# Kernel optimization log

Measured on AMD Instinct MI355X. Metric: run time of the kernel, lower is better.

The kernel has to match this reference:

```python
import jax, jax.numpy as jnp
import numpy as np

IMG, P, CIN, D, K, L, H, FF, B = 512, 32, 3, 256, 8192, 6, 8, 1024, 32
GRID = IMG // P  # 16
DH = D // H
EPS = 1e-5


def _ln(x, w, b):
    m = x.mean(-1, keepdims=True)
    v = ((x - m) ** 2).mean(-1, keepdims=True)
    return (x - m) / jnp.sqrt(v + EPS) * w + b


def _mha(x, wqkv, bqkv, wo, bo):
    # x: (S, Bt, D) -- axis 0 is the attention axis (torch batch_first=False quirk)
    S, Bt, _ = x.shape
    qkv = x @ wqkv.T + bqkv
    q, k, v = jnp.split(qkv, 3, axis=-1)
    q = q.reshape(S, Bt, H, DH)
    k = k.reshape(S, Bt, H, DH)
    v = v.reshape(S, Bt, H, DH)
    scores = jnp.einsum('sbhd,tbhd->bhst', q, k) / jnp.sqrt(jnp.float32(DH))
    attn = jax.nn.softmax(scores, axis=-1)
    o = jnp.einsum('bhst,tbhd->sbhd', attn, v).reshape(S, Bt, D)
    return o @ wo.T + bo


def _conv_t(x, w, b, stride=2, pad=1):
    # w uses torch ConvTranspose2d layout (Cin, Cout, kH, kW)
    kH = w.shape[2]
    wf = jnp.flip(w, (2, 3)).transpose(1, 0, 2, 3)  # -> (Cout, Cin, kH, kW)
    y = jax.lax.conv_general_dilated(
        x, wf, window_strides=(1, 1),
        padding=[(kH - 1 - pad, kH - 1 - pad)] * 2,
        lhs_dilation=(stride, stride),
        dimension_numbers=('NCHW', 'OIHW', 'NCHW'))
    return y + b[None, :, None, None]


def _forward(x, patch_w, patch_b, qkv_w, qkv_b, out_w, out_b, ln1_w, ln1_b,
             ln2_w, ln2_b, ff1_w, ff1_b, ff2_w, ff2_b, lnf_w, lnf_b, codebook,
             dec_w0, dec_b0, dec_w1, dec_b1, dec_w2, dec_b2, dec_w3, dec_b3):
    # patch embedding: conv stride=patch -> (B, D, G, G) -> (B, N, D)
    h = jax.lax.conv_general_dilated(
        x, patch_w, (P, P), 'VALID',
        dimension_numbers=('NCHW', 'OIHW', 'NCHW')) + patch_b[None, :, None, None]
    h = h.reshape(h.shape[0], D, -1).transpose(0, 2, 1)  # (B, N, D)
    # torch TransformerEncoderLayer default batch_first=False: attention runs
    # over axis 0 (image batch); faithfully replicated here. Post-norm, eval
    # mode (dropout=identity), exact gelu.
    for i in range(L):
        a = _mha(h, qkv_w[i], qkv_b[i], out_w[i], out_b[i])
        h = _ln(h + a, ln1_w[i], ln1_b[i])
        f = jax.nn.gelu(h @ ff1_w[i].T + ff1_b[i], approximate=False) @ ff2_w[i].T + ff2_b[i]
        h = _ln(h + f, ln2_w[i], ln2_b[i])
    h = _ln(h, lnf_w, lnf_b)
    # vector quantization: squared-distance argmin over codebook
    flat = h.reshape(-1, D)  # (B*N, D)
    d = ((flat ** 2).sum(-1, keepdims=True)
         - 2.0 * flat @ codebook.T
         + (codebook ** 2).sum(-1))  # (B*N, K)
    idx = jnp.argmin(d, axis=1)
    q = codebook[idx].reshape(h.shape)
    e_loss = jnp.mean((jax.lax.stop_gradient(q) - h) ** 2)
    q_loss = jnp.mean((q - jax.lax.stop_gradient(h)) ** 2)
    vq_loss = q_loss + 0.25 * e_loss
    q = h + jax.lax.stop_gradient(q - h)  # straight-through
    q = q.transpose(0, 2, 1).reshape(x.shape[0], D, GRID, GRID)
    y = jax.nn.relu(_conv_t(q, dec_w0, dec_b0))
    y = jax.nn.relu(_conv_t(y, dec_w1, dec_b1))
    y = jax.nn.relu(_conv_t(y, dec_w2, dec_b2))
    x_hat = jax.nn.sigmoid(_conv_t(y, dec_w3, dec_b3))
    return x_hat, vq_loss


def setup_inputs() -> dict:
    key = jax.random.key(0)
    ks = iter(jax.random.split(key, 64))
    nrm = lambda shape, s=0.02: jax.random.normal(next(ks), shape, jnp.float32) * s
    f32 = jnp.float32
    return {
        'x': jax.random.normal(next(ks), (B, CIN, IMG, IMG), f32),
        'patch_w': nrm((D, CIN, P, P)),
        'patch_b': jnp.zeros((D,), f32),
        'qkv_w': nrm((L, 3 * D, D)),
        'qkv_b': jnp.zeros((L, 3 * D), f32),
        'out_w': nrm((L, D, D)),
        'out_b': jnp.zeros((L, D), f32),
        'ln1_w': jnp.ones((L, D), f32),
        'ln1_b': jnp.zeros((L, D), f32),
        'ln2_w': jnp.ones((L, D), f32),
        'ln2_b': jnp.zeros((L, D), f32),
        'ff1_w': nrm((L, FF, D)),
        'ff1_b': jnp.zeros((L, FF), f32),
        'ff2_w': nrm((L, D, FF)),
        'ff2_b': jnp.zeros((L, D), f32),
        'lnf_w': jnp.ones((D,), f32),
        'lnf_b': jnp.zeros((D,), f32),
        'codebook': jax.random.uniform(next(ks), (K, D), f32, -1.0 / K, 1.0 / K),
        'dec_w0': nrm((D, 256, 4, 4)),
        'dec_b0': jnp.zeros((256,), f32),
        'dec_w1': nrm((256, 128, 4, 4)),
        'dec_b1': jnp.zeros((128,), f32),
        'dec_w2': nrm((128, 64, 4, 4)),
        'dec_b2': jnp.zeros((64,), f32),
        'dec_w3': nrm((64, CIN, 4, 4)),
        'dec_b3': jnp.zeros((CIN,), f32),
    }


def reference(x, patch_w, patch_b, qkv_w, qkv_b, out_w, out_b, ln1_w, ln1_b,
              ln2_w, ln2_b, ff1_w, ff1_b, ff2_w, ff2_b, lnf_w, lnf_b, codebook,
              dec_w0, dec_b0, dec_w1, dec_b1, dec_w2, dec_b2, dec_w3, dec_b3):
    return _forward(x, patch_w, patch_b, qkv_w, qkv_b, out_w, out_b, ln1_w,
                    ln1_b, ln2_w, ln2_b, ff1_w, ff1_b, ff2_w, ff2_b, lnf_w,
                    lnf_b, codebook, dec_w0, dec_b0, dec_w1, dec_b1, dec_w2,
                    dec_b2, dec_w3, dec_b3)
```

## Files before the change

### kernel.cpp

```cpp
#include <hip/hip_runtime.h>
#include <hip/hip_bf16.h>
#include <math.h>

typedef __hip_bfloat16 bf16;
typedef unsigned int u32;
typedef unsigned long long u64;
using short8 = __attribute__((ext_vector_type(8))) short;
using f32x4  = __attribute__((ext_vector_type(4))) float;

__device__ __forceinline__ float b2f(bf16 v){ return __bfloat162float(v); }
__device__ __forceinline__ bf16  f2b(float v){ return __float2bfloat16(v); }
__device__ __forceinline__ float plo(u32 u){ return __uint_as_float(u << 16); }
__device__ __forceinline__ float phi(u32 u){ return __uint_as_float(u & 0xffff0000u); }

__device__ __forceinline__ void gld16(const void* g, void* l)
{
  __builtin_amdgcn_global_load_lds(
      (const __attribute__((address_space(1))) u32*)g,
      (__attribute__((address_space(3))) u32*)l, 16, 0, 0);
}

__global__ void k_detect(const u32* probe, int* flag)
{
  if (threadIdx.x == 0 && blockIdx.x == 0)
    *flag = (*probe == 0x3F800000u) ? 0 : 1;
}

struct PPack { const void* s[25]; u32 off[26]; };
__global__ __launch_bounds__(256) void k_convall(PPack pp, bf16* P, const int* flag)
{
  const u32 i = blockIdx.x * 256 + threadIdx.x;
  if (i >= pp.off[25]) return;
  int lo = 0, hi = 25;
  while (hi - lo > 1) { const int mid = (lo + hi) >> 1; if (i >= pp.off[mid]) lo = mid; else hi = mid; }
  const u32 j = i - pp.off[lo];
  P[i] = *flag ? ((const bf16*)pp.s[lo])[j] : f2b(((const float*)pp.s[lo])[j]);
}

__global__ __launch_bounds__(256) void k_zero(u32* p, int n)
{
  const int i = blockIdx.x * 256 + threadIdx.x;
  if (i < n) p[i] = 0;
}

__global__ __launch_bounds__(128) void k_im2col(const void* x, bf16* A, const int* flag)
{
  const int m = blockIdx.y;
  const int k8 = blockIdx.x * 128 + threadIdx.x;
  const int k = k8 * 8;
  const int b = m >> 8, n = m & 255;
  const int gy = n >> 4, gx = n & 15;
  const int c = k >> 10, r = (k >> 5) & 31, pp = k & 31;
  const size_t src = (((size_t)(b * 3 + c) * 512) + gy * 32 + r) * 512 + gx * 32 + pp;
  bf16 ov[8];
  if (*flag) {
    const bf16* xp = (const bf16*)x + src;
    #pragma unroll
    for (int i = 0; i < 8; ++i) ov[i] = xp[i];
  } else {
    const float4 v0 = *reinterpret_cast<const float4*>((const float*)x + src);
    const float4 v1 = *reinterpret_cast<const float4*>((const float*)x + src + 4);
    ov[0]=f2b(v0.x); ov[1]=f2b(v0.y); ov[2]=f2b(v0.z); ov[3]=f2b(v0.w);
    ov[4]=f2b(v1.x); ov[5]=f2b(v1.y); ov[6]=f2b(v1.z); ov[7]=f2b(v1.w);
  }
  *reinterpret_cast<uint4*>(A + (size_t)m * 3072 + k) = *reinterpret_cast<const uint4*>(ov);
}

template<int EPI, int FM, bool DB>
__global__ __launch_bounds__(256, 2) void gemm_t(
    const bf16* __restrict__ A, const bf16* __restrict__ Bw,
    const bf16* __restrict__ bias, const bf16* res, bf16* C, float* __restrict__ Cf,
    const float* __restrict__ cnorm, u64* __restrict__ ku,
    int M, int N, int K, int Kc)
{
  constexpr int BM = FM * 32;
  __shared__ alignas(16) bf16 As[DB ? 2 : 1][BM * 64];
  __shared__ alignas(16) bf16 Bs[DB ? 2 : 1][128 * 64];
  const int tid = threadIdx.x;
  const int bn = blockIdx.x * 128, bm = blockIdx.y * BM;
  const int z = blockIdx.z;
  const int kb = z * Kc;
  const int l = tid & 63, w = tid >> 6;
  const int wm = w >> 1, wn = w & 1;
  const int lg = l >> 4, lr = l & 15;
  const int sr8 = l >> 3;
  const int sch = (l & 7) ^ sr8;
  f32x4 acc[FM][4];
  #pragma unroll
  for (int fm = 0; fm < FM; ++fm)
    #pragma unroll
    for (int fn = 0; fn < 4; ++fn) acc[fm][fn] = (f32x4){0.f, 0.f, 0.f, 0.f};

  auto stage = [&](int bb, int k0) {
    char* ab = (char*)As[bb];
    char* bp = (char*)Bs[bb];
    #pragma unroll
    for (int it = 0; it < FM; ++it) {
      const int r = w * 8 + it * 32 + sr8;
      gld16(A + (size_t)(bm + r) * K + k0 + sch * 8, ab + w * 1024 + it * 4096);
    }
    #pragma unroll
    for (int it = 0; it < 4; ++it) {
      const int r = w * 8 + it * 32 + sr8;
      gld16(Bw + (size_t)(bn + r) * K + k0 + sch * 8, bp + w * 1024 + it * 4096);
    }
  };
  auto compute = [&](int bb) {
    const char* ab = (const char*)As[bb];
    const char* bp = (const char*)Bs[bb];
    #pragma unroll
    for (int ks = 0; ks < 2; ++ks) {
      short8 af[FM], bfr[4];
      #pragma unroll
      for (int fm = 0; fm < FM; ++fm) {
        const int r = wm * (FM * 16) + fm * 16 + lr;
        af[fm] = *reinterpret_cast<const short8*>(ab + r * 128 + (((lg + ks * 4) ^ (r & 7)) * 16));
      }
      #pragma unroll
      for (int fn = 0; fn < 4; ++fn) {
        const int r = wn * 64 + fn * 16 + lr;
        bfr[fn] = *reinterpret_cast<const short8*>(bp + r * 128 + (((lg + ks * 4) ^ (r & 7)) * 16));
      }
      #pragma unroll
      for (int fm = 0; fm < FM; ++fm)
        #pragma unroll
        for (int fn = 0; fn < 4; ++fn)
          acc[fm][fn] = __builtin_amdgcn_mfma_f32_16x16x32_bf16(af[fm], bfr[fn], acc[fm][fn], 0, 0, 0);
    }
  };

  const int nt = Kc >> 6;
  if (DB) {
    stage(0, kb);
    __syncthreads();
    for (int t = 0; t < nt; ++t) {
      const int cur = t & 1;
      if (t + 1 < nt) stage(cur ^ 1, kb + ((t + 1) << 6));
      compute(cur);
      __syncthreads();
    }
  } else {
    for (int t = 0; t < nt; ++t) {
      if (t) __syncthreads();
      stage(0, kb + (t << 6));
      __syncthreads();
      compute(0);
    }
  }

  if (EPI == 3) {
    __shared__ u64 skey[BM][2];
    float cn4[4];
    #pragma unroll
    for (int fn = 0; fn < 4; ++fn) cn4[fn] = cnorm[bn + wn * 64 + fn * 16 + lr];
    #pragma unroll
    for (int fm = 0; fm < FM; ++fm) {
      #pragma unroll
      for (int r = 0; r < 4; ++r) {
        u64 best = ~0ull;
        #pragma unroll
        for (int fn = 0; fn < 4; ++fn) {
          const int col = bn + wn * 64 + fn * 16 + lr;
          const float d = cn4[fn] - 2.0f * acc[fm][fn][r];
          u32 u = __float_as_uint(d);
          u = (u & 0x80000000u) ? ~u : (u | 0x80000000u);
          const u64 key = ((u64)u << 32) | (u32)col;
          best = key < best ? key : best;
        }
        #pragma unroll
        for (int mk = 1; mk < 16; mk <<= 1) {
          const u64 o = __shfl_xor(best, mk, 64);
          best = o < best ? o : best;
        }
        if (lr == 0) skey[wm * (FM * 16) + fm * 16 + lg * 4 + r][wn] = best;
      }
    }
    __syncthreads();
    if (tid < BM) {
      const u64 a = skey[tid][0], b = skey[tid][1];
      ku[(size_t)blockIdx.x * M + bm + tid] = a < b ? a : b;
    }
  } else if (EPI == 4) {
    #pragma unroll
    for (int fm = 0; fm < FM; ++fm) {
      const int m0 = bm + wm * (FM * 16) + fm * 16 + lg * 4;
      #pragma unroll
      for (int fn = 0; fn < 4; ++fn) {
        const int n = bn + wn * 64 + fn * 16 + lr;
        #pragma unroll
        for (int r = 0; r < 4; ++r)
          Cf[((size_t)z * M + m0 + r) * N + n] = acc[fm][fn][r];
      }
    }
  } else {
    #pragma unroll
    for (int fm = 0; fm < FM; ++fm) {
      const int m0 = bm + wm * (FM * 16) + fm * 16 + lg * 4;
      #pragma unroll
      for (int fn = 0; fn < 4; ++fn) {
        const int n = bn + wn * 64 + fn * 16 + lr;
        const float bs = b2f(bias[n]);
        #pragma unroll
        for (int r = 0; r < 4; ++r) {
          float v = acc[fm][fn][r] + bs;
          if (EPI == 1) v = 0.5f * v * (1.0f + erff(v * 0.70710678118654752f));
          if (EPI == 2) v += b2f(res[(size_t)(m0 + r) * N + n]);
          C[(size_t)(m0 + r) * N + n] = f2b(v);
        }
      }
    }
  }
}

template<bool DOLN>
__global__ __launch_bounds__(256) void k_lnred(
    const float* __restrict__ Pf, const bf16* __restrict__ bias,
    const bf16* res, const bf16* __restrict__ lw, const bf16* __restrict__ lb,
    bf16* h, int kc)
{
  __shared__ float red[256];
  __shared__ float stat[2];
  const int row = blockIdx.x, d = threadIdx.x;
  float s = 0.f;
  for (int z = 0; z < kc; ++z) s += Pf[((size_t)z * 8192 + row) * 256 + d];
  s += b2f(bias[d]);
  if (res) s += b2f(res[(size_t)row * 256 + d]);
  if (!DOLN) { h[(size_t)row * 256 + d] = f2b(s); return; }
  red[d] = s;
  __syncthreads();
  for (int off = 128; off > 0; off >>= 1) {
    if (d < off) red[d] += red[d + off];
    __syncthreads();
  }
  if (d == 0) stat[0] = red[0] * (1.0f / 256.0f);
  __syncthreads();
  const float m = stat[0];
  red[d] = (s - m) * (s - m);
  __syncthreads();
  for (int off = 128; off > 0; off >>= 1) {
    if (d < off) red[d] += red[d + off];
    __syncthreads();
  }
  if (d == 0) stat[1] = 1.0f / sqrtf(red[0] * (1.0f / 256.0f) + 1e-5f);
  __syncthreads();
  h[(size_t)row * 256 + d] = f2b((s - m) * stat[1] * b2f(lw[d]) + b2f(lb[d]));
}

__global__ __launch_bounds__(256) void k_vqmerge(
    const u64* __restrict__ ku, int* __restrict__ idx, int M, int NB)
{
  const int r = blockIdx.x * 256 + threadIdx.x;
  if (r >= M) return;
  u64 best = ku[r];
  for (int nb = 1; nb < NB; ++nb) {
    const u64 k = ku[(size_t)nb * M + r];
    best = k < best ? k : best;
  }
  idx[r] = (int)(best & 0xFFFFFFFFull);
}

__global__ __launch_bounds__(256) void k_cnorm(const bf16* __restrict__ cb, float* __restrict__ cn)
{
  const int j = blockIdx.x * 256 + threadIdx.x;
  const u32* p = (const u32*)(cb + (size_t)j * 256);
  float s = 0.f;
  for (int k = 0; k < 128; ++k) {
    const u32 v = p[k];
    const float a = plo(v), b = phi(v);
    s += a * a + b * b;
  }
  cn[j] = s;
}

__global__ __launch_bounds__(256) void k_ln(
    bf16* h, const bf16* w, const bf16* b)
{
  __shared__ float red[256];
  __shared__ float stat[2];
  const int row = blockIdx.x, d = threadIdx.x;
  const size_t base = (size_t)row * 256;
  const float x = b2f(h[base + d]);
  red[d] = x;
  __syncthreads();
  for (int off = 128; off > 0; off >>= 1) {
    if (d < off) red[d] += red[d + off];
    __syncthreads();
  }
  if (d == 0) stat[0] = red[0] * (1.0f / 256.0f);
  __syncthreads();
  const float m = stat[0];
  red[d] = (x - m) * (x - m);
  __syncthreads();
  for (int off = 128; off > 0; off >>= 1) {
    if (d < off) red[d] += red[d + off];
    __syncthreads();
  }
  if (d == 0) stat[1] = 1.0f / sqrtf(red[0] * (1.0f / 256.0f) + 1e-5f);
  __syncthreads();
  h[base + d] = f2b((x - m) * stat[1] * b2f(w[d]) + b2f(b[d]));
}

__global__ __launch_bounds__(256) void k_attn(
    const bf16* __restrict__ qkv, bf16* __restrict__ o)
{
  __shared__ float qs[32][33], ks[32][33], vs[32][33], ps[32][33];
  __shared__ float rs[32];
  const int bt = blockIdx.x, hd = blockIdx.y;
  const int tid = threadIdx.x;
  #pragma unroll
  for (int e = 0; e < 2; ++e) {
    const int i = tid + 256 * e;
    if (i < 384) {
      const int plane = i >> 7;
      const int rem = i & 127;
      const int s = rem >> 2, c4 = rem & 3;
      const uint4 v = *reinterpret_cast<const uint4*>(
          qkv + (size_t)(s * 256 + bt) * 768 + plane * 256 + hd * 32 + c4 * 8);
      float* dst = (plane == 0 ? &qs[s][0] : plane == 1 ? &ks[s][0] : &vs[s][0]) + c4 * 8;
      dst[0]=plo(v.x); dst[1]=phi(v.x); dst[2]=plo(v.y); dst[3]=phi(v.y);
      dst[4]=plo(v.z); dst[5]=phi(v.z); dst[6]=plo(v.w); dst[7]=phi(v.w);
    }
  }
  __syncthreads();
  const int s = tid >> 3, j = tid & 7;
  float sc[4];
  #pragma unroll
  for (int e = 0; e < 4; ++e) {
    const int t = j + 8 * e;
    float v = 0.f;
    #pragma unroll
    for (int dd = 0; dd < 32; ++dd) v += qs[s][dd] * ks[t][dd];
    sc[e] = v * 0.17677669529663687f;
  }
  float mx = fmaxf(fmaxf(sc[0], sc[1]), fmaxf(sc[2], sc[3]));
  #pragma unroll
  for (int mk = 1; mk < 8; mk <<= 1) mx = fmaxf(mx, __shfl_xor(mx, mk, 64));
  float sm = 0.f; float ex[4];
  #pragma unroll
  for (int e = 0; e < 4; ++e) { ex[e] = expf(sc[e] - mx); sm += ex[e]; }
  #pragma unroll
  for (int mk = 1; mk < 8; mk <<= 1) sm += __shfl_xor(sm, mk, 64);
  #pragma unroll
  for (int e = 0; e < 4; ++e) ps[s][j + 8 * e] = ex[e];
  if (j == 0) rs[s] = 1.0f / sm;
  __syncthreads();
  const float rinv = rs[s];
  float av[4];
  #pragma unroll
  for (int e = 0; e < 4; ++e) {
    const int dd = j * 4 + e;
    float acc = 0.f;
    #pragma unroll
    for (int t = 0; t < 32; ++t) acc += ps[s][t] * vs[t][dd];
    av[e] = acc * rinv;
  }
  alignas(8) bf16 ov[4];
  #pragma unroll
  for (int e = 0; e < 4; ++e) ov[e] = f2b(av[e]);
  *reinterpret_cast<ushort4*>(o + (size_t)(s * 256 + bt) * 256 + hd * 32 + j * 4) =
      *reinterpret_cast<const ushort4*>(ov);
}

__global__ __launch_bounds__(256) void k_gather(
    const bf16* h, const bf16* cb, const int* idx, bf16* a0, float* lsum)
{
  __shared__ float red[256];
  const int row = blockIdx.x, d = threadIdx.x;
  const int code = idx[row] & 8191;
  const float q = b2f(cb[(size_t)code * 256 + d]);
  const float x = b2f(h[(size_t)row * 256 + d]);
  red[d] = (q - x) * (q - x);
  __syncthreads();
  for (int off = 128; off > 0; off >>= 1) {
    if (d < off) red[d] += red[d + off];
    __syncthreads();
  }
  if (d == 0) lsum[row] = red[0];
  const int b = row >> 8, n = row & 255;
  const int y = n >> 4, xc = n & 15;
  a0[(((size_t)b * 18 + y + 1) * 18 + (xc + 1)) * 256 + d] = f2b(q);
}

__global__ __launch_bounds__(256) void k_loss(const float* lsum, float* out)
{
  __shared__ float red[256];
  const int tid = threadIdx.x;
  float v = 0.f;
  for (int i = 0; i < 32; ++i) v += lsum[tid + 256 * i];
  red[tid] = v;
  __syncthreads();
  for (int off = 128; off > 0; off >>= 1) {
    if (tid < off) red[tid] += red[tid + off];
    __syncthreads();
  }
  if (tid == 0)
    out[0] = red[0] * (1.25f / 2097152.0f);
}

__global__ __launch_bounds__(256) void k_wtrans(
    const bf16* __restrict__ w, bf16* __restrict__ wt,
    int Cin, int lCin, int CoutR, int CoutP)
{
  const int K = Cin << 2;
  const int total = 4 * CoutP * K;
  const int i = blockIdx.x * 256 + threadIdx.x;
  if (i >= total) return;
  const int p = i / (CoutP * K);
  const int rem = i - p * (CoutP * K);
  const int co = rem / K;
  const int k = rem - co * K;
  const int tap = k >> lCin, ci = k - (tap << lCin);
  const int py = p >> 1, px = p & 1, ty = tap >> 1, tx = tap & 1;
  bf16 v = f2b(0.f);
  if (co < CoutR)
    v = w[(((size_t)ci * CoutR + co) * 4 + py + 2 * ty) * 4 + px + 2 * tx];
  wt[i] = v;
}

__global__ __launch_bounds__(256, 2) void convt64(
    const bf16* __restrict__ in, const bf16* __restrict__ Wt,
    const bf16* __restrict__ bias, bf16* __restrict__ outp,
    int H, int lH, int Cin, int lCin, int Cout)
{
  __shared__ alignas(16) bf16 As[2][128 * 64];
  __shared__ alignas(16) bf16 Bs[2][64 * 64];
  const int tid = threadIdx.x;
  const int pz = blockIdx.z;
  const int py = pz >> 1, px = pz & 1;
  const int K = Cin << 2;
  const int bn = blockIdx.x * 64, bm = blockIdx.y * 128;
  const bf16* Bw = Wt + (size_t)pz * Cout * K;
  const int l = tid & 63, w = tid >> 6;
  const int wm = w >> 1, wn = w & 1;
  const int lg = l >> 4, lr = l & 15;
  const int sr8 = l >> 3;
  const int sch = (l & 7) ^ sr8;
  const int Hp = H + 2;
  f32x4 acc[4][2];
  #pragma unroll
  for (int fm = 0; fm < 4; ++fm)
    #pragma unroll
    for (int fn = 0; fn < 2; ++fn) acc[fm][fn] = (f32x4){0.f, 0.f, 0.f, 0.f};

  size_t pixbase[4];
  #pragma unroll
  for (int it = 0; it < 4; ++it) {
    const int m = bm + w * 8 + it * 32 + sr8;
    const int b = m >> (2 * lH);
    const int rem = m & ((1 << (2 * lH)) - 1);
    const int jj = rem >> lH, ii = rem & (H - 1);
    pixbase[it] = ((size_t)(b * Hp + jj) * Hp + ii);
  }

  auto stage = [&](int bb, int k0) {
    char* ab = (char*)As[bb];
    char* bp = (char*)Bs[bb];
    const int tap = k0 >> lCin;
    const int ty = tap >> 1, tx = tap & 1;
    const int sy = (1 - py) + (1 - ty);
    const int sx = (1 - px) + (1 - tx);
    const int ci0 = (k0 - (tap << lCin)) + sch * 8;
    #pragma unroll
    for (int it = 0; it < 4; ++it)
      gld16(in + (pixbase[it] + (size_t)sy * Hp + sx) * Cin + ci0,
            ab + w * 1024 + it * 4096);
    #pragma unroll
    for (int it = 0; it < 2; ++it) {
      const int r = w * 8 + it * 32 + sr8;
      gld16(Bw + (size_t)(bn + r) * K + k0 + sch * 8, bp + w * 1024 + it * 4096);
    }
  };

  const int nt = K >> 6;
  stage(0, 0);
  __syncthreads();
  for (int t = 0; t < nt; ++t) {
    const int cur = t & 1;
    if (t + 1 < nt) stage(cur ^ 1, (t + 1) << 6);
    const char* ab = (const char*)As[cur];
    const char* bb = (const char*)Bs[cur];
    #pragma unroll
    for (int ks = 0; ks < 2; ++ks) {
      short8 af[4], bfr[2];
      #pragma unroll
      for (int fm = 0; fm < 4; ++fm) {
        const int r = wm * 64 + fm * 16 + lr;
        af[fm] = *reinterpret_cast<const short8*>(ab + r * 128 + (((lg + ks * 4) ^ (r & 7)) * 16));
      }
      #pragma unroll
      for (int fn = 0; fn < 2; ++fn) {
        const int r = wn * 32 + fn * 16 + lr;
        bfr[fn] = *reinterpret_cast<const short8*>(bb + r * 128 + (((lg + ks * 4) ^ (r & 7)) * 16));
      }
      #pragma unroll
      for (int fm = 0; fm < 4; ++fm)
        #pragma unroll
        for (int fn = 0; fn < 2; ++fn)
          acc[fm][fn] = __builtin_amdgcn_mfma_f32_16x16x32_bf16(af[fm], bfr[fn], acc[fm][fn], 0, 0, 0);
    }
    __syncthreads();
  }

  const int Ho = 2 * H, Hop = Ho + 2;
  #pragma unroll
  for (int fm = 0; fm < 4; ++fm) {
    const int m0 = bm + wm * 64 + fm * 16 + lg * 4;
    #pragma unroll
    for (int fn = 0; fn < 2; ++fn) {
      const int n = bn + wn * 32 + fn * 16 + lr;
      #pragma unroll
      for (int r = 0; r < 4; ++r) {
        const int m = m0 + r;
        const int b = m >> (2 * lH);
        const int rem = m & ((1 << (2 * lH)) - 1);
        const int jj = rem >> lH, ii = rem & (H - 1);
        const int oy = 2 * jj + (1 - py), ox = 2 * ii + (1 - px);
        const float v = fmaxf(acc[fm][fn][r] + b2f(bias[n]), 0.f);
        outp[((size_t)(b * Hop + oy + 1) * Hop + ox + 1) * Cout + n] = f2b(v);
      }
    }
  }
}

__global__ __launch_bounds__(256) void k_dec3(
    const bf16* __restrict__ a3, const bf16* __restrict__ wt3,
    const bf16* __restrict__ bias, float* __restrict__ xhat, int chunkBase)
{
  __shared__ float wl[3][264];
  const int tid = threadIdx.x;
  const int pz = blockIdx.y;
  const int py = pz >> 1, px = pz & 1;
  for (int i = tid; i < 768; i += 256) {
    const int co = i >> 8, k = i & 255;
    wl[co][k] = b2f(wt3[(pz * 3 + co) * 256 + k]);
  }
  __syncthreads();
  const int b = blockIdx.z;
  const int p = blockIdx.x * 64 + (tid >> 2);
  const int jj = p >> 7, ii = p & 127;
  const int ch4 = tid & 3;
  float a0 = 0.f, a1 = 0.f, a2 = 0.f;
  #pragma unroll
  for (int ty = 0; ty < 2; ++ty) {
    #pragma unroll
    for (int tx = 0; tx < 2; ++tx) {
      const int sy = (1 - py) + (1 - ty), sx = (1 - px) + (1 - tx);
      const int tap = ty * 2 + tx;
      const u32* ip = (const u32*)(a3 + ((size_t)(b * 130 + jj + sy) * 130 + ii + sx) * 64) + ch4 * 8;
      const float* w0 = &wl[0][tap * 64 + ch4 * 16];
      const float* w1 = &wl[1][tap * 64 + ch4 * 16];
      const float* w2 = &wl[2][tap * 64 + ch4 * 16];
      #pragma unroll
      for (int kk = 0; kk < 8; ++kk) {
        const u32 v = ip[kk];
        const float e0 = plo(v), e1 = phi(v);
        a0 += e0 * w0[2 * kk] + e1 * w0[2 * kk + 1];
        a1 += e0 * w1[2 * kk] + e1 * w1[2 * kk + 1];
        a2 += e0 * w2[2 * kk] + e1 * w2[2 * kk + 1];
      }
    }
  }
  a0 += __shfl_xor(a0, 1, 64); a0 += __shfl_xor(a0, 2, 64);
  a1 += __shfl_xor(a1, 1, 64); a1 += __shfl_xor(a1, 2, 64);
  a2 += __shfl_xor(a2, 1, 64); a2 += __shfl_xor(a2, 2, 64);
  if (ch4 < 3) {
    const float av = ch4 == 0 ? a0 : (ch4 == 1 ? a1 : a2);
    const int oy = 2 * jj + (1 - py), ox = 2 * ii + (1 - px);
    const float t = av + b2f(bias[ch4]);
    xhat[(((size_t)(chunkBase + b) * 3 + ch4) * 256 + oy) * 256 + ox] =
        1.0f / (1.0f + expf(-t));
  }
}

extern "C" void kernel_launch(void* const* d_in, const int* in_sizes, int n_in,
                              void* d_out, int out_size, void* d_ws, size_t ws_size,
                              hipStream_t stream)
{
  float* xhat = (float*)d_out;
  float* lossout = xhat + (out_size - 1);

  const size_t NEED = 130195456;
  if (ws_size < NEED) return;

  char* ws = (char*)d_ws;
  int*   flag  = (int*)  (ws + 0);
  float* lsum  = (float*)(ws + 1024);
  int*   idx   = (int*)  (ws + 65536);
  u64*   ku    = (u64*)  (ws + 131072);
  bf16*  P     = (bf16*) (ws + 8519680);
  bf16*  WT    = (bf16*) (ws + 27262976);
  float* cnorm = (float*)(ws + 30900224);
  bf16*  hbuf  = (bf16*) (ws + 31457280);
  bf16*  A_im  = (bf16*) (ws + 35651584);
  bf16*  qkvb  = (bf16*) (ws + 35651584);
  bf16*  obuf  = (bf16*) (ws + 48234496);
  bf16*  ffb   = (bf16*) (ws + 52428800);
  float* Pf    = (float*)(ws + 85983232);
  bf16*  a0    = (bf16*) (ws + 35651584);
  bf16*  a1    = (bf16*) (ws + 40960000);
  bf16*  a2    = (bf16*) (ws + 59899904);
  bf16*  a3    = (bf16*) (ws + 95584256);

  k_detect<<<1, 64, 0, stream>>>((const u32*)d_in[7], flag);

  size_t poff[26]; poff[1] = 0;
  for (int i = 2; i <= 25; ++i) poff[i] = poff[i - 1] + (size_t)in_sizes[i - 1];
  const size_t ptotal = poff[25] + (size_t)in_sizes[25];
  PPack pp;
  for (int i = 0; i < 25; ++i) { pp.s[i] = d_in[i + 1]; pp.off[i] = (u32)poff[i + 1]; }
  pp.off[25] = (u32)ptotal;
  k_convall<<<(int)((ptotal + 255) / 256), 256, 0, stream>>>(pp, P, flag);

  const bf16 *patch_w = P + poff[1],  *patch_b = P + poff[2];
  const bf16 *qkv_w   = P + poff[3],  *qkv_b   = P + poff[4];
  const bf16 *out_w   = P + poff[5],  *out_b   = P + poff[6];
  const bf16 *ln1_w   = P + poff[7],  *ln1_b   = P + poff[8];
  const bf16 *ln2_w   = P + poff[9],  *ln2_b   = P + poff[10];
  const bf16 *ff1_w   = P + poff[11], *ff1_b   = P + poff[12];
  const bf16 *ff2_w   = P + poff[13], *ff2_b   = P + poff[14];
  const bf16 *lnf_w   = P + poff[15], *lnf_b   = P + poff[16];
  const bf16 *codebook= P + poff[17];
  const bf16 *dec_w0  = P + poff[18], *dec_b0  = P + poff[19];
  const bf16 *dec_w1  = P + poff[20], *dec_b1  = P + poff[21];
  const bf16 *dec_w2  = P + poff[22], *dec_b2  = P + poff[23];
  const bf16 *dec_w3  = P + poff[24], *dec_b3  = P + poff[25];

  bf16* wt0 = WT;
  bf16* wt1 = wt0 + 1048576;
  bf16* wt2 = wt1 + 524288;
  bf16* wt3 = wt2 + 131072;
  k_wtrans<<<(1048576 + 255) / 256, 256, 0, stream>>>(dec_w0, wt0, 256, 8, 256, 256);
  k_wtrans<<<(524288 + 255) / 256, 256, 0, stream>>>(dec_w1, wt1, 256, 8, 128, 128);
  k_wtrans<<<(131072 + 255) / 256, 256, 0, stream>>>(dec_w2, wt2, 128, 7, 64, 64);
  k_wtrans<<<(3072 + 255) / 256, 256, 0, stream>>>(dec_w3, wt3, 64, 6, 3, 3);
  k_cnorm<<<32, 256, 0, stream>>>(codebook, cnorm);

  k_im2col<<<dim3(3, 8192), 128, 0, stream>>>(d_in[0], A_im, flag);
  gemm_t<4, 2, true><<<dim3(2, 128, 4), 256, 0, stream>>>(
      A_im, patch_w, nullptr, nullptr, nullptr, Pf, nullptr, nullptr, 8192, 256, 3072, 768);
  k_lnred<false><<<8192, 256, 0, stream>>>(
      Pf, patch_b, nullptr, nullptr, nullptr, hbuf, 4);

  for (int l = 0; l < 6; ++l) {
    gemm_t<0, 2, false><<<dim3(6, 128, 1), 256, 0, stream>>>(
        hbuf, qkv_w + (size_t)l * 768 * 256, qkv_b + l * 768, nullptr, qkvb, nullptr,
        nullptr, nullptr, 8192, 768, 256, 256);
    k_attn<<<dim3(256, 8), 256, 0, stream>>>(qkvb, obuf);
    gemm_t<2, 2, false><<<dim3(2, 128, 1), 256, 0, stream>>>(
        obuf, out_w + (size_t)l * 256 * 256, out_b + l * 256, hbuf, hbuf, nullptr,
        nullptr, nullptr, 8192, 256, 256, 256);
    k_ln<<<8192, 256, 0, stream>>>(hbuf, ln1_w + l * 256, ln1_b + l * 256);
    gemm_t<1, 2, false><<<dim3(8, 128, 1), 256, 0, stream>>>(
        hbuf, ff1_w + (size_t)l * 1024 * 256, ff1_b + l * 1024, nullptr, ffb, nullptr,
        nullptr, nullptr, 8192, 1024, 256, 256);
    gemm_t<4, 2, false><<<dim3(2, 128, 4), 256, 0, stream>>>(
        ffb, ff2_w + (size_t)l * 256 * 1024, nullptr, nullptr, nullptr, Pf,
        nullptr, nullptr, 8192, 256, 1024, 256);
    k_lnred<true><<<8192, 256, 0, stream>>>(
        Pf, ff2_b + l * 256, hbuf, ln2_w + l * 256, ln2_b + l * 256, hbuf, 4);
  }
  k_ln<<<8192, 256, 0, stream>>>(hbuf, lnf_w, lnf_b);

  gemm_t<3, 2, false><<<dim3(64, 128, 1), 256, 0, stream>>>(
      hbuf, codebook, nullptr, nullptr, nullptr, nullptr, cnorm, ku, 8192, 8192, 256, 256);
  k_vqmerge<<<32, 256, 0, stream>>>(ku, idx, 8192, 64);

  k_zero<<<(1327104 + 255) / 256, 256, 0, stream>>>((u32*)a0, 1327104);
  k_gather<<<8192, 256, 0, stream>>>(hbuf, codebook, idx, a0, lsum);
  k_loss<<<1, 256, 0, stream>>>(lsum, lossout);

  k_zero<<<(4734976 + 255) / 256, 256, 0, stream>>>((u32*)a1, 4734976);
  k_zero<<<(8921088 + 255) / 256, 256, 0, stream>>>((u32*)a2, 8921088);
  k_zero<<<(8652800 + 255) / 256, 256, 0, stream>>>((u32*)a3, 8652800);

  convt64<<<dim3(4, 64, 4), 256, 0, stream>>>(a0, wt0, dec_b0, a1, 16, 4, 256, 8, 256);
  convt64<<<dim3(2, 256, 4), 256, 0, stream>>>(a1, wt1, dec_b1, a2, 32, 5, 256, 8, 128);
  for (int c = 0; c < 2; ++c) {
    const bf16* a2c = a2 + (size_t)c * 16 * 66 * 66 * 128;
    convt64<<<dim3(1, 512, 4), 256, 0, stream>>>(a2c, wt2, dec_b2, a3, 64, 6, 128, 7, 64);
    k_dec3<<<dim3(256, 4, 16), 256, 0, stream>>>(a3, wt3, dec_b3, xhat, c * 16);
  }
}
```

Baseline: 1.019 ms.

## Zero only padding borders, store split-K partials in bf16, widen GEMM N tiles

Full-buffer zeroing of the padded decoder activations is replaced by a kernel that writes zeros only to the one-pixel border, assuming the interior is fully overwritten. Split-K partial sums for the patch embedding and FF2 GEMMs are now stored in bf16 instead of fp32, halving that write and reread traffic at some cost in accumulation precision. The GEMM gains a BN template parameter, and the QKV, FF1 and VQ-distance GEMMs use 256-wide N tiles, which halves their grid size and doubles per-block accumulator registers.

```diff
diff --git a/kernel.cpp b/kernel.cpp
--- a/kernel.cpp
+++ b/kernel.cpp
@@ -37,10 +37,28 @@
   P[i] = *flag ? ((const bf16*)pp.s[lo])[j] : f2b(((const float*)pp.s[lo])[j]);
 }
 
-__global__ __launch_bounds__(256) void k_zero(u32* p, int n)
-{
+__global__ __launch_bounds__(256) void k_zborder(bf16* buf, int Hp, int C, int nimg)
+{
+  const int per = 4 * Hp - 4;
+  const int c8 = C >> 3;
+  const int total = nimg * per * c8;
   const int i = blockIdx.x * 256 + threadIdx.x;
-  if (i < n) p[i] = 0;
+  if (i >= total) return;
+  const int ch8 = i % c8;
+  const int pb = i / c8;
+  const int img = pb / per;
+  const int b = pb - img * per;
+  int y, x;
+  if (b < Hp) { y = 0; x = b; }
+  else if (b < 2 * Hp) { y = Hp - 1; x = b - Hp; }
+  else {
+    const int r = b - 2 * Hp;
+    const int side = r / (Hp - 2);
+    y = 1 + r - side * (Hp - 2);
+    x = side ? (Hp - 1) : 0;
+  }
+  uint4 z = {0, 0, 0, 0};
+  *reinterpret_cast<uint4*>(buf + (((size_t)img * Hp + y) * Hp + x) * C + ch8 * 8) = z;
 }
 
 __global__ __launch_bounds__(128) void k_im2col(const void* x, bf16* A, const int* flag)
@@ -66,18 +84,19 @@
   *reinterpret_cast<uint4*>(A + (size_t)m * 3072 + k) = *reinterpret_cast<const uint4*>(ov);
 }
 
-template<int EPI, int FM, bool DB>
+template<int EPI, int FM, int BN, bool DB>
 __global__ __launch_bounds__(256, 2) void gemm_t(
     const bf16* __restrict__ A, const bf16* __restrict__ Bw,
-    const bf16* __restrict__ bias, const bf16* res, bf16* C, float* __restrict__ Cf,
+    const bf16* __restrict__ bias, const bf16* res, bf16* C,
     const float* __restrict__ cnorm, u64* __restrict__ ku,
     int M, int N, int K, int Kc)
 {
   constexpr int BM = FM * 32;
+  constexpr int FN = BN / 32;
   __shared__ alignas(16) bf16 As[DB ? 2 : 1][BM * 64];
-  __shared__ alignas(16) bf16 Bs[DB ? 2 : 1][128 * 64];
+  __shared__ alignas(16) bf16 Bs[DB ? 2 : 1][BN * 64];
   const int tid = threadIdx.x;
-  const int bn = blockIdx.x * 128, bm = blockIdx.y * BM;
+  const int bn = blockIdx.x * BN, bm = blockIdx.y * BM;
   const int z = blockIdx.z;
   const int kb = z * Kc;
   const int l = tid & 63, w = tid >> 6;
@@ -85,11 +104,11 @@
   const int lg = l >> 4, lr = l & 15;
   const int sr8 = l >> 3;
   const int sch = (l & 7) ^ sr8;
-  f32x4 acc[FM][4];
+  f32x4 acc[FM][FN];
   #pragma unroll
   for (int fm = 0; fm < FM; ++fm)
     #pragma unroll
-    for (int fn = 0; fn < 4; ++fn) acc[fm][fn] = (f32x4){0.f, 0.f, 0.f, 0.f};
+    for (int fn = 0; fn < FN; ++fn) acc[fm][fn] = (f32x4){0.f, 0.f, 0.f, 0.f};
 
   auto stage = [&](int bb, int k0) {
     char* ab = (char*)As[bb];
@@ -100,7 +119,7 @@
       gld16(A + (size_t)(bm + r) * K + k0 + sch * 8, ab + w * 1024 + it * 4096);
     }
     #pragma unroll
-    for (int it = 0; it < 4; ++it) {
+    for (int it = 0; it < BN / 32; ++it) {
       const int r = w * 8 + it * 32 + sr8;
       gld16(Bw + (size_t)(bn + r) * K + k0 + sch * 8, bp + w * 1024 + it * 4096);
     }
@@ -110,21 +129,21 @@
     const char* bp = (const char*)Bs[bb];
     #pragma unroll
     for (int ks = 0; ks < 2; ++ks) {
-      short8 af[FM], bfr[4];
+      short8 af[FM], bfr[FN];
       #pragma unroll
       for (int fm = 0; fm < FM; ++fm) {
         const int r = wm * (FM * 16) + fm * 16 + lr;
         af[fm] = *reinterpret_cast<const short8*>(ab + r * 128 + (((lg + ks * 4) ^ (r & 7)) * 16));
       }
       #pragma unroll
-      for (int fn = 0; fn < 4; ++fn) {
-        const int r = wn * 64 + fn * 16 + lr;
+      for (int fn = 0; fn < FN; ++fn) {
+        const int r = wn * (BN / 2) + fn * 16 + lr;
         bfr[fn] = *reinterpret_cast<const short8*>(bp + r * 128 + (((lg + ks * 4) ^ (r & 7)) * 16));
       }
       #pragma unroll
       for (int fm = 0; fm < FM; ++fm)
         #pragma unroll
-        for (int fn = 0; fn < 4; ++fn)
+        for (int fn = 0; fn < FN; ++fn)
           acc[fm][fn] = __builtin_amdgcn_mfma_f32_16x16x32_bf16(af[fm], bfr[fn], acc[fm][fn], 0, 0, 0);
     }
   };
@@ -150,18 +169,18 @@
 
   if (EPI == 3) {
     __shared__ u64 skey[BM][2];
-    float cn4[4];
-    #pragma unroll
-    for (int fn = 0; fn < 4; ++fn) cn4[fn] = cnorm[bn + wn * 64 + fn * 16 + lr];
+    float cn[FN];
+    #pragma unroll
+    for (int fn = 0; fn < FN; ++fn) cn[fn] = cnorm[bn + wn * (BN / 2) + fn * 16 + lr];
     #pragma unroll
     for (int fm = 0; fm < FM; ++fm) {
       #pragma unroll
       for (int r = 0; r < 4; ++r) {
         u64 best = ~0ull;
         #pragma unroll
-        for (int fn = 0; fn < 4; ++fn) {
-          const int col = bn + wn * 64 + fn * 16 + lr;
-          const float d = cn4[fn] - 2.0f * acc[fm][fn][r];
+        for (int fn = 0; fn < FN; ++fn) {
+          const int col = bn + wn * (BN / 2) + fn * 16 + lr;
+          const float d = cn[fn] - 2.0f * acc[fm][fn][r];
           u32 u = __float_as_uint(d);
           u = (u & 0x80000000u) ? ~u : (u | 0x80000000u);
           const u64 key = ((u64)u << 32) | (u32)col;
@@ -185,11 +204,11 @@
     for (int fm = 0; fm < FM; ++fm) {
       const int m0 = bm + wm * (FM * 16) + fm * 16 + lg * 4;
       #pragma unroll
-      for (int fn = 0; fn < 4; ++fn) {
-        const int n = bn + wn * 64 + fn * 16 + lr;
+      for (int fn = 0; fn < FN; ++fn) {
+        const int n = bn + wn * (BN / 2) + fn * 16 + lr;
         #pragma unroll
         for (int r = 0; r < 4; ++r)
-          Cf[((size_t)z * M + m0 + r) * N + n] = acc[fm][fn][r];
+          C[((size_t)z * M + m0 + r) * N + n] = f2b(acc[fm][fn][r]);
       }
     }
   } else {
@@ -197,8 +216,8 @@
     for (int fm = 0; fm < FM; ++fm) {
       const int m0 = bm + wm * (FM * 16) + fm * 16 + lg * 4;
       #pragma unroll
-      for (int fn = 0; fn < 4; ++fn) {
-        const int n = bn + wn * 64 + fn * 16 + lr;
+      for (int fn = 0; fn < FN; ++fn) {
+        const int n = bn + wn * (BN / 2) + fn * 16 + lr;
         const float bs = b2f(bias[n]);
         #pragma unroll
         for (int r = 0; r < 4; ++r) {
@@ -214,7 +233,7 @@
 
 template<bool DOLN>
 __global__ __launch_bounds__(256) void k_lnred(
-    const float* __restrict__ Pf, const bf16* __restrict__ bias,
+    const bf16* __restrict__ Pf, const bf16* __restrict__ bias,
     const bf16* res, const bf16* __restrict__ lw, const bf16* __restrict__ lb,
     bf16* h, int kc)
 {
@@ -222,7 +241,7 @@
   __shared__ float stat[2];
   const int row = blockIdx.x, d = threadIdx.x;
   float s = 0.f;
-  for (int z = 0; z < kc; ++z) s += Pf[((size_t)z * 8192 + row) * 256 + d];
+  for (int z = 0; z < kc; ++z) s += b2f(Pf[((size_t)z * 8192 + row) * 256 + d]);
   s += b2f(bias[d]);
   if (res) s += b2f(res[(size_t)row * 256 + d]);
   if (!DOLN) { h[(size_t)row * 256 + d] = f2b(s); return; }
@@ -595,7 +614,7 @@
   bf16*  qkvb  = (bf16*) (ws + 35651584);
   bf16*  obuf  = (bf16*) (ws + 48234496);
   bf16*  ffb   = (bf16*) (ws + 52428800);
-  float* Pf    = (float*)(ws + 85983232);
+  bf16*  Pfb   = (bf16*) (ws + 85983232);
   bf16*  a0    = (bf16*) (ws + 35651584);
   bf16*  a1    = (bf16*) (ws + 40960000);
   bf16*  a2    = (bf16*) (ws + 59899904);
@@ -636,42 +655,41 @@
   k_cnorm<<<32, 256, 0, stream>>>(codebook, cnorm);
 
   k_im2col<<<dim3(3, 8192), 128, 0, stream>>>(d_in[0], A_im, flag);
-  gemm_t<4, 2, true><<<dim3(2, 128, 4), 256, 0, stream>>>(
-      A_im, patch_w, nullptr, nullptr, nullptr, Pf, nullptr, nullptr, 8192, 256, 3072, 768);
+  gemm_t<4, 2, 128, true><<<dim3(2, 128, 4), 256, 0, stream>>>(
+      A_im, patch_w, nullptr, nullptr, Pfb, nullptr, nullptr, 8192, 256, 3072, 768);
   k_lnred<false><<<8192, 256, 0, stream>>>(
-      Pf, patch_b, nullptr, nullptr, nullptr, hbuf, 4);
+      Pfb, patch_b, nullptr, nullptr, nullptr, hbuf, 4);
 
   for (int l = 0; l < 6; ++l) {
-    gemm_t<0, 2, false><<<dim3(6, 128, 1), 256, 0, stream>>>(
-        hbuf, qkv_w + (size_t)l * 768 * 256, qkv_b + l * 768, nullptr, qkvb, nullptr,
+    gemm_t<0, 2, 256, false><<<dim3(3, 128, 1), 256, 0, stream>>>(
+        hbuf, qkv_w + (size_t)l * 768 * 256, qkv_b + l * 768, nullptr, qkvb,
         nullptr, nullptr, 8192, 768, 256, 256);
     k_attn<<<dim3(256, 8), 256, 0, stream>>>(qkvb, obuf);
-    gemm_t<2, 2, false><<<dim3(2, 128, 1), 256, 0, stream>>>(
-        obuf, out_w + (size_t)l * 256 * 256, out_b + l * 256, hbuf, hbuf, nullptr,
+    gemm_t<2, 2, 128, false><<<dim3(2, 128, 1), 256, 0, stream>>>(
+        obuf, out_w + (size_t)l * 256 * 256, out_b + l * 256, hbuf, hbuf,
         nullptr, nullptr, 8192, 256, 256, 256);
     k_ln<<<8192, 256, 0, stream>>>(hbuf, ln1_w + l * 256, ln1_b + l * 256);
-    gemm_t<1, 2, false><<<dim3(8, 128, 1), 256, 0, stream>>>(
-        hbuf, ff1_w + (size_t)l * 1024 * 256, ff1_b + l * 1024, nullptr, ffb, nullptr,
+    gemm_t<1, 2, 256, false><<<dim3(4, 128, 1), 256, 0, stream>>>(
+        hbuf, ff1_w + (size_t)l * 1024 * 256, ff1_b + l * 1024, nullptr, ffb,
         nullptr, nullptr, 8192, 1024, 256, 256);
-    gemm_t<4, 2, false><<<dim3(2, 128, 4), 256, 0, stream>>>(
-        ffb, ff2_w + (size_t)l * 256 * 1024, nullptr, nullptr, nullptr, Pf,
+    gemm_t<4, 2, 128, false><<<dim3(2, 128, 4), 256, 0, stream>>>(
+        ffb, ff2_w + (size_t)l * 256 * 1024, nullptr, nullptr, Pfb,
         nullptr, nullptr, 8192, 256, 1024, 256);
     k_lnred<true><<<8192, 256, 0, stream>>>(
-        Pf, ff2_b + l * 256, hbuf, ln2_w + l * 256, ln2_b + l * 256, hbuf, 4);
+        Pfb, ff2_b + l * 256, hbuf, ln2_w + l * 256, ln2_b + l * 256, hbuf, 4);
   }
   k_ln<<<8192, 256, 0, stream>>>(hbuf, lnf_w, lnf_b);
 
-  gemm_t<3, 2, false><<<dim3(64, 128, 1), 256, 0, stream>>>(
-      hbuf, codebook, nullptr, nullptr, nullptr, nullptr, cnorm, ku, 8192, 8192, 256, 256);
-  k_vqmerge<<<32, 256, 0, stream>>>(ku, idx, 8192, 64);
-
-  k_zero<<<(1327104 + 255) / 256, 256, 0, stream>>>((u32*)a0, 1327104);
+  gemm_t<3, 2, 256, false><<<dim3(32, 128, 1), 256, 0, stream>>>(
+      hbuf, codebook, nullptr, nullptr, nullptr, cnorm, ku, 8192, 8192, 256, 256);
+  k_vqmerge<<<32, 256, 0, stream>>>(ku, idx, 8192, 32);
+
+  k_zborder<<<(32 * 68 * 32 + 255) / 256, 256, 0, stream>>>(a0, 18, 256, 32);
   k_gather<<<8192, 256, 0, stream>>>(hbuf, codebook, idx, a0, lsum);
   k_loss<<<1, 256, 0, stream>>>(lsum, lossout);
-
-  k_zero<<<(4734976 + 255) / 256, 256, 0, stream>>>((u32*)a1, 4734976);
-  k_zero<<<(8921088 + 255) / 256, 256, 0, stream>>>((u32*)a2, 8921088);
-  k_zero<<<(8652800 + 255) / 256, 256, 0, stream>>>((u32*)a3, 8652800);
+  k_zborder<<<(32 * 132 * 32 + 255) / 256, 256, 0, stream>>>(a1, 34, 256, 32);
+  k_zborder<<<(32 * 260 * 16 + 255) / 256, 256, 0, stream>>>(a2, 66, 128, 32);
+  k_zborder<<<(16 * 516 * 8 + 255) / 256, 256, 0, stream>>>(a3, 130, 64, 16);
 
   convt64<<<dim3(4, 64, 4), 256, 0, stream>>>(a0, wt0, dec_b0, a1, 16, 4, 256, 8, 256);
   convt64<<<dim3(2, 256, 4), 256, 0, stream>>>(a1, wt1, dec_b1, a2, 32, 5, 256, 8, 128);
```

Result: no change. 1.002 ms (-1.7%).
